# Kernel tuning notes

Measured on AMD Instinct MI355X. Metric: run time of the kernel, lower is better.

Reference implementation:

```python
import jax, jax.numpy as jnp
import numpy as np

N_EMBD = 2048
N_HEAD = 16
N_KV_HEAD = 4
HEAD_DIM = 128
KV_REPEATS = N_HEAD // N_KV_HEAD
ROPE_THETA = 10000.0


def rotate_half(x):
    # interleaved pair rotation: (x0,x1,x2,x3,...) -> (-x1,x0,-x3,x2,...)
    x_even = x[..., 0::2]
    x_odd = x[..., 1::2]
    return jnp.stack((-x_odd, x_even), axis=-1).reshape(x.shape)


def apply_rope(q, k, position_ids):
    inv_freq = 1.0 / (ROPE_THETA ** (jnp.arange(0, HEAD_DIM, 2, dtype=jnp.float32) / HEAD_DIM))
    freqs = position_ids.astype(jnp.float32)[:, None] * inv_freq[None, :]  # [S, D/2]
    emb = jnp.repeat(freqs, 2, axis=-1)  # [S, D] interleaved
    cos = jnp.cos(emb)[None, None, :, :]
    sin = jnp.sin(emb)[None, None, :, :]
    return q * cos + rotate_half(q) * sin, k * cos + rotate_half(k) * sin


def setup_inputs() -> dict:
    key = jax.random.key(0)
    ks = jax.random.split(key, 5)
    B, S = 2, 2048
    x = jax.random.normal(ks[0], (B, S, N_EMBD), dtype=jnp.float32)
    position_ids = jnp.arange(S, dtype=jnp.int32)
    scale = 0.02
    Wq = jax.random.normal(ks[1], (N_HEAD * HEAD_DIM, N_EMBD), dtype=jnp.float32) * scale
    Wk = jax.random.normal(ks[2], (N_KV_HEAD * HEAD_DIM, N_EMBD), dtype=jnp.float32) * scale
    Wv = jax.random.normal(ks[3], (N_KV_HEAD * HEAD_DIM, N_EMBD), dtype=jnp.float32) * scale
    Wo = jax.random.normal(ks[4], (N_EMBD, N_EMBD), dtype=jnp.float32) * scale
    return {"x": x, "Wq": Wq, "Wk": Wk, "Wv": Wv, "Wo": Wo, "position_ids": position_ids}


def reference(x, Wq, Wk, Wv, Wo, position_ids):
    B, S, _ = x.shape
    q = (x @ Wq.T).reshape(B, S, N_HEAD, HEAD_DIM).transpose(0, 2, 1, 3)      # [B,H,S,D]
    k = (x @ Wk.T).reshape(B, S, N_KV_HEAD, HEAD_DIM).transpose(0, 2, 1, 3)  # [B,Hkv,S,D]
    v = (x @ Wv.T).reshape(B, S, N_KV_HEAD, HEAD_DIM).transpose(0, 2, 1, 3)
    q, k = apply_rope(q, k, position_ids)
    # GQA: repeat kv heads consecutively
    k = jnp.repeat(k, KV_REPEATS, axis=1)  # [B,H,S,D]
    v = jnp.repeat(v, KV_REPEATS, axis=1)
    scores = jnp.einsum('bhqd,bhkd->bhqk', q, k) / jnp.sqrt(jnp.asarray(HEAD_DIM, q.dtype))
    key_positions = jnp.arange(S)
    mask = key_positions[None, :] > position_ids[:, None]  # [S, S]
    scores = jnp.where(mask[None, None, :, :], jnp.finfo(scores.dtype).min, scores)
    weights = jax.nn.softmax(scores.astype(jnp.float32), axis=-1).astype(q.dtype)
    y = jnp.einsum('bhqk,bhkd->bhqd', weights, v)
    y = y.transpose(0, 2, 1, 3).reshape(B, S, N_EMBD)
    return y @ Wo.T
```

## Files before the change

### kernel.cpp

```cpp
#include <hip/hip_runtime.h>
#include <stdint.h>

typedef unsigned short u16;
typedef unsigned int   u32;
typedef __attribute__((ext_vector_type(8))) short short8;
typedef __attribute__((ext_vector_type(4))) float f32x4;

#define S_LEN 2048
#define NEMB  2048
#define NH    16
#define NKV   4
#define HD    128
#define BATCH 2
#define MROWS (BATCH*S_LEN)

__device__ __forceinline__ u16 f2bf(float f){
  u32 u = __float_as_uint(f);
  u += 0x7fffu + ((u>>16)&1u);
  return (u16)(u>>16);
}
__device__ __forceinline__ float bf2f(u16 h){
  return __uint_as_float(((u32)h)<<16);
}

typedef __attribute__((address_space(1))) const void gc_void;
typedef __attribute__((address_space(3))) void lds_void;
__device__ __forceinline__ void load_lds16(const void* g, void* l){
  __builtin_amdgcn_global_load_lds((gc_void*)(uintptr_t)g,
      (lds_void*)(u32)(uintptr_t)l, 16, 0, 0);
}

__global__ __launch_bounds__(256) void convert_kernel(
    const float* __restrict__ x, const float* __restrict__ wq,
    const float* __restrict__ wk, const float* __restrict__ wv,
    const float* __restrict__ wo,
    u16* __restrict__ xb, u16* __restrict__ wcb, u16* __restrict__ wob){
  const size_t NX=2097152, NWQ=1048576, NWK=262144, NWV=262144, NWO=1048576;
  const size_t total = NX+NWQ+NWK+NWV+NWO;
  for (size_t i = (size_t)blockIdx.x*blockDim.x + threadIdx.x; i < total;
       i += (size_t)gridDim.x*blockDim.x){
    const float* src; u16* dst; size_t j = i;
    if (j < NX){ src=x; dst=xb; }
    else { j-=NX;
      if (j<NWQ){ src=wq; dst=wcb; }
      else { j-=NWQ;
        if (j<NWK){ src=wk; dst=wcb+4194304; }
        else { j-=NWK;
          if (j<NWV){ src=wv; dst=wcb+5242880; }
          else { j-=NWV; src=wo; dst=wob; } } } }
    float4 v = *(const float4*)(src + j*4);
    u32 lo = (u32)f2bf(v.x) | ((u32)f2bf(v.y)<<16);
    u32 hi = (u32)f2bf(v.z) | ((u32)f2bf(v.w)<<16);
    uint2 pk; pk.x = lo; pk.y = hi;
    *(uint2*)(dst + j*4) = pk;
  }
}

__global__ __launch_bounds__(256) void rope_table_kernel(const int* __restrict__ pos,
                                                         float* __restrict__ tab){
  int id = blockIdx.x*256 + threadIdx.x;
  if (id >= S_LEN*64) return;
  int s = id >> 6, i = id & 63;
  float p = (float)pos[s];
  float inv = __expf(-((float)(2*i)) * (1.0f/128.0f) * 9.210340371976184f);
  float f = p * inv;
  float sv, cv;
  sincosf(f, &sv, &cv);
  tab[id*2]   = cv;
  tab[id*2+1] = sv;
}

__global__ __launch_bounds__(256) void rope_apply_kernel(u16* __restrict__ buf,
    const float* __restrict__ tab, int cols, int cshift, float scale){
  int nch = MROWS * (cols>>3);
  int stride = gridDim.x*blockDim.x;
  for (int ch = blockIdx.x*blockDim.x + threadIdx.x; ch < nch; ch += stride){
    int m   = ch >> cshift;
    int cc  = ch & ((1<<cshift)-1);
    int col = cc<<3;
    int d   = col & (HD-1);
    int i0  = d >> 1;
    int s   = m & (S_LEN-1);
    const float* tp = tab + (size_t)(s*64 + i0)*2;
    float4 t0 = *(const float4*)tp;
    float4 t1 = *(const float4*)(tp+4);
    u16* bp = buf + (size_t)m*cols + col;
    union { uint4 v; u16 e[8]; } U, O;
    U.v = *(const uint4*)bp;
    float a, b;
    a=bf2f(U.e[0]); b=bf2f(U.e[1]);
    O.e[0]=f2bf((a*t0.x - b*t0.y)*scale); O.e[1]=f2bf((b*t0.x + a*t0.y)*scale);
    a=bf2f(U.e[2]); b=bf2f(U.e[3]);
    O.e[2]=f2bf((a*t0.z - b*t0.w)*scale); O.e[3]=f2bf((b*t0.z + a*t0.w)*scale);
    a=bf2f(U.e[4]); b=bf2f(U.e[5]);
    O.e[4]=f2bf((a*t1.x - b*t1.y)*scale); O.e[5]=f2bf((b*t1.x + a*t1.y)*scale);
    a=bf2f(U.e[6]); b=bf2f(U.e[7]);
    O.e[6]=f2bf((a*t1.z - b*t1.w)*scale); O.e[7]=f2bf((b*t1.z + a*t1.w)*scale);
    *(uint4*)bp = O.v;
  }
}

__global__ __launch_bounds__(256) void transpose_v_kernel(const u16* __restrict__ vb,
                                                          u16* __restrict__ vt){
  __shared__ u16 tl[64][72];
  int bx = blockIdx.x;
  int m0 = (bx & 63)*64;
  int d0 = (bx >> 6)*64;
  int tid = threadIdx.x;
  #pragma unroll
  for (int i=0;i<2;i++){
    int t16 = i*256 + tid;
    int sl = t16 >> 3, dc = t16 & 7;
    *(uint4*)&tl[sl][dc*8] = *(const uint4*)&vb[(size_t)(m0+sl)*512 + d0 + dc*8];
  }
  __syncthreads();
  #pragma unroll
  for (int i=0;i<2;i++){
    int t16 = i*256 + tid;
    int sch = t16 >> 6, dl = t16 & 63;
    union { uint4 v; u16 e[8]; } O;
    #pragma unroll
    for (int j=0;j<8;j++) O.e[j] = tl[sch*8+j][dl];
    *(uint4*)&vt[(size_t)(d0+dl)*4096 + m0 + sch*8] = O.v;
  }
}

template<int EPI>
__global__ __launch_bounds__(256,2) void gemm128_kernel(
    const u16* __restrict__ A, const u16* __restrict__ B, int K,
    u16* __restrict__ q_out, u16* __restrict__ k_out, u16* __restrict__ v_out,
    float* __restrict__ f_out){
  __shared__ u16 sA[2][128*32];
  __shared__ u16 sB[2][128*32];
  int tid = threadIdx.x;
  int wave = tid >> 6, lane = tid & 63;
  int lr = lane & 15, lc = lane >> 4;
  int wm = (wave>>1)*64, wn = (wave&1)*64;
  int bm = blockIdx.y*128, bn = blockIdx.x*128;
  const u16* Ag = A + (size_t)bm*K;
  const u16* Bg = B + (size_t)bn*K;

  auto stage = [&](int buf, int kt){
    const u16* Ak = Ag + kt*32;
    const u16* Bk = Bg + kt*32;
    #pragma unroll
    for (int rrd=0; rrd<2; ++rrd){
      int t16 = rrd*256 + tid;
      int row = t16 >> 2, ch = t16 & 3;
      u16* lb = &sA[buf][(size_t)(rrd*256 + (tid & 192))*8];
      load_lds16(Ak + (size_t)row*K + ch*8, lb);
    }
    #pragma unroll
    for (int rrd=0; rrd<2; ++rrd){
      int t16 = rrd*256 + tid;
      int row = t16 >> 2, ch = t16 & 3;
      u16* lb = &sB[buf][(size_t)(rrd*256 + (tid & 192))*8];
      load_lds16(Bk + (size_t)row*K + ch*8, lb);
    }
  };

  f32x4 acc[4][4];
  #pragma unroll
  for (int i=0;i<4;i++)
    #pragma unroll
    for (int j=0;j<4;j++) acc[i][j] = (f32x4)0.0f;

  stage(0,0);
  __syncthreads();
  int nk = K >> 5;
  int cur = 0;
  for (int kt=0; kt<nk; ++kt){
    if (kt+1 < nk) stage(cur^1, kt+1);
    short8 af[4], bfr[4];
    #pragma unroll
    for (int i=0;i<4;i++){
      af[i]  = *(const short8*)&sA[cur][(wm + i*16 + lr)*32 + lc*8];
      bfr[i] = *(const short8*)&sB[cur][(wn + i*16 + lr)*32 + lc*8];
    }
    __builtin_amdgcn_s_setprio(1);
    #pragma unroll
    for (int i=0;i<4;i++)
      #pragma unroll
      for (int j=0;j<4;j++)
        acc[i][j] = __builtin_amdgcn_mfma_f32_16x16x32_bf16(af[i], bfr[j], acc[i][j], 0,0,0);
    __builtin_amdgcn_s_setprio(0);
    __syncthreads();
    cur ^= 1;
  }

  #pragma unroll
  for (int i=0;i<4;i++){
    #pragma unroll
    for (int j=0;j<4;j++){
      #pragma unroll
      for (int r=0;r<4;r++){
        int m = bm + wm + i*16 + lc*4 + r;
        int n = bn + wn + j*16 + lr;
        float v = acc[i][j][r];
        if (EPI == 0){
          if (n < 2048)      q_out[(size_t)m*2048 + n]        = f2bf(v);
          else if (n < 2560) k_out[(size_t)m*512 + (n-2048)]  = f2bf(v);
          else               v_out[(size_t)m*512 + (n-2560)]  = f2bf(v);
        } else {
          f_out[(size_t)m*2048 + n] = v;
        }
      }
    }
  }
}

__global__ __launch_bounds__(256,2) void attn_kernel(
    const u16* __restrict__ Q, const u16* __restrict__ Kb,
    const u16* __restrict__ Vt, u16* __restrict__ Y){
  __shared__ u16 sK[2][64*128];
  __shared__ u16 sVt[2][128*64];
  __shared__ u16 sP[4][16*64];

  int tid = threadIdx.x, wave = tid>>6, lane = tid&63;
  int lr = lane&15, lc = lane>>4;

  int bid = blockIdx.x;
  int kvg  = bid & 7;
  int rest = bid >> 3;
  int qtr  = rest & 31;
  int hsub = rest >> 5;
  int qt = 31 - qtr;
  int b  = kvg >> 2;
  int hk = kvg & 3;
  int h  = hk*4 + hsub;

  int q0  = qt*64;
  int qrb = q0 + wave*16;
  const u16* Qg = Q  + (size_t)(b*S_LEN + qrb)*NEMB + h*HD;
  const u16* Kg = Kb + (size_t)(b*S_LEN)*512 + hk*HD;
  const u16* Vg = Vt + (size_t)(hk*HD)*4096 + b*S_LEN;

  auto stage = [&](int buf, int kv0){
    #pragma unroll
    for (int i=0;i<4;i++){
      int t16 = i*256 + tid;
      int row = t16 >> 4, c = t16 & 15;
      int cgl = c ^ (row & 7);
      load_lds16(Kg + (size_t)(kv0+row)*512 + cgl*8,
                 &sK[buf][(size_t)(i*256 + (tid & 192))*8]);
    }
    #pragma unroll
    for (int i=0;i<4;i++){
      int t16 = i*256 + tid;
      int d = t16 >> 3, c = t16 & 7;
      int cgl = c ^ (d & 7);
      load_lds16(Vg + (size_t)d*4096 + kv0 + cgl*8,
                 &sVt[buf][(size_t)(i*256 + (tid & 192))*8]);
    }
  };

  short8 qf[4];
  #pragma unroll
  for (int c=0;c<4;c++)
    qf[c] = *(const short8*)&Qg[(size_t)lr*NEMB + c*32 + lc*8];

  float m_run[4], l_run[4];
  #pragma unroll
  for (int r=0;r<4;r++){ m_run[r]=-1e30f; l_run[r]=0.0f; }
  f32x4 o[8];
  #pragma unroll
  for (int i=0;i<8;i++) o[i]=(f32x4)0.0f;

  int nt = qt + 1;
  stage(0,0);
  __syncthreads();
  int cur=0;
  char* spb = (char*)sP[wave];
  for (int t=0;t<nt;++t){
    int kv0 = t*64;
    if (t+1<nt) stage(cur^1,(t+1)*64);

    f32x4 sc[4];
    #pragma unroll
    for (int c2=0;c2<4;c2++) sc[c2]=(f32x4)0.0f;
    const char* skb = (const char*)sK[cur];
    __builtin_amdgcn_s_setprio(1);
    #pragma unroll
    for (int c2=0;c2<4;c2++){
      int rr = c2*16 + lr;
      int xo = (rr&7)<<4;
      #pragma unroll
      for (int c=0;c<4;c++){
        int byteoff = (rr*256 + c*64 + lc*16) ^ xo;
        short8 kf = *(const short8*)(skb + byteoff);
        sc[c2] = __builtin_amdgcn_mfma_f32_16x16x32_bf16(qf[c], kf, sc[c2], 0,0,0);
      }
    }
    __builtin_amdgcn_s_setprio(0);

    if (t == nt-1){
      #pragma unroll
      for (int c2=0;c2<4;c2++){
        int kvgl = kv0 + c2*16 + lr;
        #pragma unroll
        for (int r=0;r<4;r++){
          int qg = qrb + lc*4 + r;
          if (kvgl > qg) sc[c2][r] = -1e30f;
        }
      }
    }

    float fac[4];
    #pragma unroll
    for (int r=0;r<4;r++){
      float mm = fmaxf(fmaxf(sc[0][r],sc[1][r]), fmaxf(sc[2][r],sc[3][r]));
      mm = fmaxf(mm, __shfl_xor(mm,1));
      mm = fmaxf(mm, __shfl_xor(mm,2));
      mm = fmaxf(mm, __shfl_xor(mm,4));
      mm = fmaxf(mm, __shfl_xor(mm,8));
      float mn = fmaxf(m_run[r], mm);
      fac[r] = __expf(m_run[r]-mn);
      m_run[r] = mn;
      float p0 = __expf(sc[0][r]-mn);
      float p1 = __expf(sc[1][r]-mn);
      float p2 = __expf(sc[2][r]-mn);
      float p3 = __expf(sc[3][r]-mn);
      sc[0][r]=p0; sc[1][r]=p1; sc[2][r]=p2; sc[3][r]=p3;
      float ss = (p0+p1)+(p2+p3);
      ss += __shfl_xor(ss,1); ss += __shfl_xor(ss,2);
      ss += __shfl_xor(ss,4); ss += __shfl_xor(ss,8);
      l_run[r] = l_run[r]*fac[r] + ss;
    }
    #pragma unroll
    for (int i=0;i<8;i++)
      #pragma unroll
      for (int r=0;r<4;r++) o[i][r] *= fac[r];

    #pragma unroll
    for (int c2=0;c2<4;c2++){
      #pragma unroll
      for (int r=0;r<4;r++){
        int row = lc*4+r;
        int byteoff = (row*128 + (c2*16+lr)*2) ^ ((row&7)<<4);
        *(u16*)(spb + byteoff) = f2bf(sc[c2][r]);
      }
    }
    short8 pa[2];
    {
      int xop = (lr&7)<<4;
      pa[0] = *(const short8*)(spb + ((lr*128 + lc*16) ^ xop));
      pa[1] = *(const short8*)(spb + ((lr*128 + 64 + lc*16) ^ xop));
    }

    const char* svb = (const char*)sVt[cur];
    __builtin_amdgcn_s_setprio(1);
    #pragma unroll
    for (int n=0;n<8;n++){
      int d = n*16+lr;
      int xo = (d&7)<<4;
      #pragma unroll
      for (int ks=0;ks<2;ks++){
        int byteoff = (d*128 + ks*64 + lc*16) ^ xo;
        short8 vf = *(const short8*)(svb + byteoff);
        o[n] = __builtin_amdgcn_mfma_f32_16x16x32_bf16(pa[ks], vf, o[n], 0,0,0);
      }
    }
    __builtin_amdgcn_s_setprio(0);

    __syncthreads();
    cur ^= 1;
  }

  u16* Yg = Y + (size_t)(b*S_LEN + qrb)*NEMB + h*HD;
  #pragma unroll
  for (int n=0;n<8;n++){
    #pragma unroll
    for (int r=0;r<4;r++){
      float v = o[n][r] / l_run[r];
      Yg[(size_t)(lc*4+r)*NEMB + n*16 + lr] = f2bf(v);
    }
  }
}

extern "C" void kernel_launch(void* const* d_in, const int* in_sizes, int n_in,
                              void* d_out, int out_size, void* d_ws, size_t ws_size,
                              hipStream_t stream){
  const float* x  = (const float*)d_in[0];
  const float* wq = (const float*)d_in[1];
  const float* wk = (const float*)d_in[2];
  const float* wv = (const float*)d_in[3];
  const float* wo = (const float*)d_in[4];
  const int*  pos = (const int*)d_in[5];
  float* out = (float*)d_out;

  char* ws = (char*)d_ws;
  size_t off = 0;
  auto alloc = [&](size_t bytes)->char*{
    char* p = ws + off; off += (bytes + 255) & ~(size_t)255; return p;
  };
  u16* xb  = (u16*)alloc(8388608ull*2);
  u16* wcb = (u16*)alloc(6291456ull*2);
  u16* wob = (u16*)alloc(4194304ull*2);
  u16* qb  = (u16*)alloc(8388608ull*2);
  u16* kb  = (u16*)alloc(2097152ull*2);
  u16* vb  = (u16*)alloc(2097152ull*2);
  u16* yb  = (u16*)alloc(8388608ull*2);
  float* tab = (float*)alloc((size_t)S_LEN*64*2*4);
  u16* vt = xb;

  convert_kernel<<<2048,256,0,stream>>>(x,wq,wk,wv,wo,xb,wcb,wob);
  rope_table_kernel<<<512,256,0,stream>>>(pos, tab);
  gemm128_kernel<0><<<dim3(24,32),256,0,stream>>>(xb, wcb, 2048, qb, kb, vb, nullptr);
  rope_apply_kernel<<<2048,256,0,stream>>>(qb, tab, 2048, 8, 0.08838834764831845f);
  rope_apply_kernel<<<1024,256,0,stream>>>(kb, tab, 512, 6, 1.0f);
  transpose_v_kernel<<<512,256,0,stream>>>(vb, vt);
  attn_kernel<<<1024,256,0,stream>>>(qb, kb, vt, yb);
  gemm128_kernel<1><<<dim3(16,32),256,0,stream>>>(yb, wob, 2048, nullptr,nullptr,nullptr, out);
}
```

Measured before the change: 360.6 us.

## Replace 128x128 GEMM with 256x256 tiled, swizzled, quarter-pipelined GEMM

After: 386.0 us. 1.07x slower.

```diff
diff --git a/kernel.cpp b/kernel.cpp
--- a/kernel.cpp
+++ b/kernel.cpp
@@ -126,77 +126,170 @@
 }
 
 template<int EPI>
-__global__ __launch_bounds__(256,2) void gemm128_kernel(
-    const u16* __restrict__ A, const u16* __restrict__ B, int K,
+__global__ __launch_bounds__(512,1) void gemm256_kernel(
+    const u16* __restrict__ A, const u16* __restrict__ B, int K, int ntx,
     u16* __restrict__ q_out, u16* __restrict__ k_out, u16* __restrict__ v_out,
     float* __restrict__ f_out){
-  __shared__ u16 sA[2][128*32];
-  __shared__ u16 sB[2][128*32];
+  __shared__ char ldsb[131072];
   int tid = threadIdx.x;
-  int wave = tid >> 6, lane = tid & 63;
+  int lane = tid & 63;
+  int wid  = tid >> 6;
   int lr = lane & 15, lc = lane >> 4;
-  int wm = (wave>>1)*64, wn = (wave&1)*64;
-  int bm = blockIdx.y*128, bn = blockIdx.x*128;
+  int wm2 = wid >> 2;
+  int wn4 = wid & 3;
+
+  int nwg = ntx * 16;
+  int bid = blockIdx.x;
+  int wg = (bid & 7)*(nwg >> 3) + (bid >> 3);
+  int by = wg / ntx, bx = wg % ntx;
+  int bm = by*256, bn = bx*256;
+
   const u16* Ag = A + (size_t)bm*K;
   const u16* Bg = B + (size_t)bn*K;
 
-  auto stage = [&](int buf, int kt){
-    const u16* Ak = Ag + kt*32;
-    const u16* Bk = Bg + kt*32;
-    #pragma unroll
-    for (int rrd=0; rrd<2; ++rrd){
-      int t16 = rrd*256 + tid;
-      int row = t16 >> 2, ch = t16 & 3;
-      u16* lb = &sA[buf][(size_t)(rrd*256 + (tid & 192))*8];
-      load_lds16(Ak + (size_t)row*K + ch*8, lb);
-    }
-    #pragma unroll
-    for (int rrd=0; rrd<2; ++rrd){
-      int t16 = rrd*256 + tid;
-      int row = t16 >> 2, ch = t16 & 3;
-      u16* lb = &sB[buf][(size_t)(rrd*256 + (tid & 192))*8];
-      load_lds16(Bk + (size_t)row*K + ch*8, lb);
+  auto stageA = [&](int p, int kt, int h){
+    const u16* src = Ag + (size_t)kt*64;
+    char* dstb = ldsb + p*32768 + h*16384 + (size_t)(tid & 448)*16;
+    #pragma unroll
+    for (int i=0;i<2;i++){
+      int S = i*512 + tid;
+      int rr = S >> 3;
+      int r  = ((rr>>6)<<7) | (h<<6) | (rr & 63);
+      int c8 = (S & 7) ^ (rr & 7);
+      load_lds16(src + (size_t)r*K + c8*8, dstb + i*8192);
     }
   };
-
-  f32x4 acc[4][4];
-  #pragma unroll
-  for (int i=0;i<4;i++)
+  auto stageB = [&](int p, int kt, int h){
+    const u16* src = Bg + (size_t)kt*64;
+    char* dstb = ldsb + 65536 + p*32768 + h*16384 + (size_t)(tid & 448)*16;
+    #pragma unroll
+    for (int i=0;i<2;i++){
+      int S = i*512 + tid;
+      int rr = S >> 3;
+      int n  = ((rr>>5)<<6) | (h<<5) | (rr & 31);
+      int c8 = (S & 7) ^ (rr & 7);
+      load_lds16(src + (size_t)n*K + c8*8, dstb + i*8192);
+    }
+  };
+
+  f32x4 acc[8][4];
+  #pragma unroll
+  for (int i=0;i<8;i++)
     #pragma unroll
     for (int j=0;j<4;j++) acc[i][j] = (f32x4)0.0f;
 
-  stage(0,0);
-  __syncthreads();
-  int nk = K >> 5;
-  int cur = 0;
-  for (int kt=0; kt<nk; ++kt){
-    if (kt+1 < nk) stage(cur^1, kt+1);
-    short8 af[4], bfr[4];
-    #pragma unroll
-    for (int i=0;i<4;i++){
-      af[i]  = *(const short8*)&sA[cur][(wm + i*16 + lr)*32 + lc*8];
-      bfr[i] = *(const short8*)&sB[cur][(wn + i*16 + lr)*32 + lc*8];
-    }
+  short8 a[4][2], b0[2][2], b1[2][2];
+  int xorv = (lr & 7) << 4;
+
+  #define RD_A(mh, mf, kk, p) \
+    (*(const short8*)(ldsb + (p)*32768 + (mh)*16384 + wm2*8192 + \
+      ((((mf)*16 + lr)*128 + (kk)*64 + lc*16) ^ xorv)))
+  #define RD_B(nh, nf, kk, p) \
+    (*(const short8*)(ldsb + 65536 + (p)*32768 + (nh)*16384 + wn4*4096 + \
+      ((((nf)*16 + lr)*128 + (kk)*64 + lc*16) ^ xorv)))
+
+  int nk = K >> 6;
+
+  stageA(0, 0, 0);
+  stageB(0, 0, 0);
+  stageB(0, 0, 1);
+  stageA(0, 0, 1);
+  asm volatile("s_waitcnt vmcnt(4)" ::: "memory");
+  __builtin_amdgcn_s_barrier();
+
+  for (int t = 0; t < nk; ++t){
+    int p = t & 1;
+    bool doStage = (t+1 < nk);
+
+    #pragma unroll
+    for (int mf=0; mf<4; mf++){
+      a[mf][0] = RD_A(0, mf, 0, p);
+      a[mf][1] = RD_A(0, mf, 1, p);
+    }
+    #pragma unroll
+    for (int nf=0; nf<2; nf++){
+      b0[nf][0] = RD_B(0, nf, 0, p);
+      b0[nf][1] = RD_B(0, nf, 1, p);
+    }
+    if (doStage) stageA(p^1, t+1, 0);
+    __builtin_amdgcn_s_barrier();
     __builtin_amdgcn_s_setprio(1);
     #pragma unroll
-    for (int i=0;i<4;i++)
-      #pragma unroll
-      for (int j=0;j<4;j++)
-        acc[i][j] = __builtin_amdgcn_mfma_f32_16x16x32_bf16(af[i], bfr[j], acc[i][j], 0,0,0);
+    for (int kk=0; kk<2; kk++)
+      #pragma unroll
+      for (int mf=0; mf<4; mf++)
+        #pragma unroll
+        for (int nf=0; nf<2; nf++)
+          acc[mf][nf] = __builtin_amdgcn_mfma_f32_16x16x32_bf16(a[mf][kk], b0[nf][kk], acc[mf][nf], 0,0,0);
     __builtin_amdgcn_s_setprio(0);
-    __syncthreads();
-    cur ^= 1;
-  }
-
-  #pragma unroll
-  for (int i=0;i<4;i++){
-    #pragma unroll
-    for (int j=0;j<4;j++){
-      #pragma unroll
-      for (int r=0;r<4;r++){
-        int m = bm + wm + i*16 + lc*4 + r;
-        int n = bn + wn + j*16 + lr;
-        float v = acc[i][j][r];
+    if (doStage) { asm volatile("s_waitcnt vmcnt(4)" ::: "memory"); }
+    else         { asm volatile("s_waitcnt vmcnt(2)" ::: "memory"); }
+    __builtin_amdgcn_s_barrier();
+
+    #pragma unroll
+    for (int nf=0; nf<2; nf++){
+      b1[nf][0] = RD_B(1, nf, 0, p);
+      b1[nf][1] = RD_B(1, nf, 1, p);
+    }
+    if (doStage) stageB(p^1, t+1, 0);
+    __builtin_amdgcn_s_barrier();
+    __builtin_amdgcn_s_setprio(1);
+    #pragma unroll
+    for (int kk=0; kk<2; kk++)
+      #pragma unroll
+      for (int mf=0; mf<4; mf++)
+        #pragma unroll
+        for (int nf=0; nf<2; nf++)
+          acc[mf][2+nf] = __builtin_amdgcn_mfma_f32_16x16x32_bf16(a[mf][kk], b1[nf][kk], acc[mf][2+nf], 0,0,0);
+    __builtin_amdgcn_s_setprio(0);
+    if (doStage) { asm volatile("s_waitcnt vmcnt(4)" ::: "memory"); }
+    else         { asm volatile("s_waitcnt vmcnt(0)" ::: "memory"); }
+    __builtin_amdgcn_s_barrier();
+
+    #pragma unroll
+    for (int mf=0; mf<4; mf++){
+      a[mf][0] = RD_A(1, mf, 0, p);
+      a[mf][1] = RD_A(1, mf, 1, p);
+    }
+    if (doStage) stageB(p^1, t+1, 1);
+    __builtin_amdgcn_s_barrier();
+    __builtin_amdgcn_s_setprio(1);
+    #pragma unroll
+    for (int kk=0; kk<2; kk++)
+      #pragma unroll
+      for (int mf=0; mf<4; mf++)
+        #pragma unroll
+        for (int nf=0; nf<2; nf++)
+          acc[4+mf][nf] = __builtin_amdgcn_mfma_f32_16x16x32_bf16(a[mf][kk], b0[nf][kk], acc[4+mf][nf], 0,0,0);
+    __builtin_amdgcn_s_setprio(0);
+    __builtin_amdgcn_s_barrier();
+
+    if (doStage) stageA(p^1, t+1, 1);
+    __builtin_amdgcn_s_barrier();
+    __builtin_amdgcn_s_setprio(1);
+    #pragma unroll
+    for (int kk=0; kk<2; kk++)
+      #pragma unroll
+      for (int mf=0; mf<4; mf++)
+        #pragma unroll
+        for (int nf=0; nf<2; nf++)
+          acc[4+mf][2+nf] = __builtin_amdgcn_mfma_f32_16x16x32_bf16(a[mf][kk], b1[nf][kk], acc[4+mf][2+nf], 0,0,0);
+    __builtin_amdgcn_s_setprio(0);
+    if (doStage) { asm volatile("s_waitcnt vmcnt(4)" ::: "memory"); }
+    __builtin_amdgcn_s_barrier();
+  }
+  #undef RD_A
+  #undef RD_B
+
+  #pragma unroll
+  for (int mfi=0; mfi<8; mfi++){
+    #pragma unroll
+    for (int nfi=0; nfi<4; nfi++){
+      #pragma unroll
+      for (int r=0; r<4; r++){
+        int m = bm + wm2*128 + mfi*16 + lc*4 + r;
+        int n = bn + wn4*64 + nfi*16 + lr;
+        float v = acc[mfi][nfi][r];
         if (EPI == 0){
           if (n < 2048)      q_out[(size_t)m*2048 + n]        = f2bf(v);
           else if (n < 2560) k_out[(size_t)m*512 + (n-2048)]  = f2bf(v);
@@ -405,10 +498,10 @@
 
   convert_kernel<<<2048,256,0,stream>>>(x,wq,wk,wv,wo,xb,wcb,wob);
   rope_table_kernel<<<512,256,0,stream>>>(pos, tab);
-  gemm128_kernel<0><<<dim3(24,32),256,0,stream>>>(xb, wcb, 2048, qb, kb, vb, nullptr);
+  gemm256_kernel<0><<<192,512,0,stream>>>(xb, wcb, 2048, 12, qb, kb, vb, nullptr);
   rope_apply_kernel<<<2048,256,0,stream>>>(qb, tab, 2048, 8, 0.08838834764831845f);
   rope_apply_kernel<<<1024,256,0,stream>>>(kb, tab, 512, 6, 1.0f);
   transpose_v_kernel<<<512,256,0,stream>>>(vb, vt);
   attn_kernel<<<1024,256,0,stream>>>(qb, kb, vt, yb);
-  gemm128_kernel<1><<<dim3(16,32),256,0,stream>>>(yb, wob, 2048, nullptr,nullptr,nullptr, out);
-}
+  gemm256_kernel<1><<<128,512,0,stream>>>(yb, wob, 2048, 8, nullptr,nullptr,nullptr, out);
+}
```

## Fuse RoPE into QKV GEMM epilogue and use exp2 with lazy softmax rescaling

Applied to the files above, without the earlier changes.

Result: faster. 349.3 us (-3.1%).

```diff
diff --git a/kernel.cpp b/kernel.cpp
--- a/kernel.cpp
+++ b/kernel.cpp
@@ -14,6 +14,8 @@
 #define BATCH 2
 #define MROWS (BATCH*S_LEN)
 
+#define SCALE_Q 0.12751744f
+
 __device__ __forceinline__ u16 f2bf(float f){
   u32 u = __float_as_uint(f);
   u += 0x7fffu + ((u>>16)&1u);
@@ -21,6 +23,11 @@
 }
 __device__ __forceinline__ float bf2f(u16 h){
   return __uint_as_float(((u32)h)<<16);
+}
+__device__ __forceinline__ float exp2_fast(float x){
+  float r;
+  asm("v_exp_f32 %0, %1" : "=v"(r) : "v"(x));
+  return r;
 }
 
 typedef __attribute__((address_space(1))) const void gc_void;
@@ -57,7 +64,7 @@
 }
 
 __global__ __launch_bounds__(256) void rope_table_kernel(const int* __restrict__ pos,
-                                                         float* __restrict__ tab){
+                                                         float2* __restrict__ tab){
   int id = blockIdx.x*256 + threadIdx.x;
   if (id >= S_LEN*64) return;
   int s = id >> 6, i = id & 63;
@@ -66,38 +73,7 @@
   float f = p * inv;
   float sv, cv;
   sincosf(f, &sv, &cv);
-  tab[id*2]   = cv;
-  tab[id*2+1] = sv;
-}
-
-__global__ __launch_bounds__(256) void rope_apply_kernel(u16* __restrict__ buf,
-    const float* __restrict__ tab, int cols, int cshift, float scale){
-  int nch = MROWS * (cols>>3);
-  int stride = gridDim.x*blockDim.x;
-  for (int ch = blockIdx.x*blockDim.x + threadIdx.x; ch < nch; ch += stride){
-    int m   = ch >> cshift;
-    int cc  = ch & ((1<<cshift)-1);
-    int col = cc<<3;
-    int d   = col & (HD-1);
-    int i0  = d >> 1;
-    int s   = m & (S_LEN-1);
-    const float* tp = tab + (size_t)(s*64 + i0)*2;
-    float4 t0 = *(const float4*)tp;
-    float4 t1 = *(const float4*)(tp+4);
-    u16* bp = buf + (size_t)m*cols + col;
-    union { uint4 v; u16 e[8]; } U, O;
-    U.v = *(const uint4*)bp;
-    float a, b;
-    a=bf2f(U.e[0]); b=bf2f(U.e[1]);
-    O.e[0]=f2bf((a*t0.x - b*t0.y)*scale); O.e[1]=f2bf((b*t0.x + a*t0.y)*scale);
-    a=bf2f(U.e[2]); b=bf2f(U.e[3]);
-    O.e[2]=f2bf((a*t0.z - b*t0.w)*scale); O.e[3]=f2bf((b*t0.z + a*t0.w)*scale);
-    a=bf2f(U.e[4]); b=bf2f(U.e[5]);
-    O.e[4]=f2bf((a*t1.x - b*t1.y)*scale); O.e[5]=f2bf((b*t1.x + a*t1.y)*scale);
-    a=bf2f(U.e[6]); b=bf2f(U.e[7]);
-    O.e[6]=f2bf((a*t1.z - b*t1.w)*scale); O.e[7]=f2bf((b*t1.z + a*t1.w)*scale);
-    *(uint4*)bp = O.v;
-  }
+  tab[id] = make_float2(cv, sv);
 }
 
 __global__ __launch_bounds__(256) void transpose_v_kernel(const u16* __restrict__ vb,
@@ -128,6 +104,7 @@
 template<int EPI>
 __global__ __launch_bounds__(256,2) void gemm128_kernel(
     const u16* __restrict__ A, const u16* __restrict__ B, int K,
+    const float2* __restrict__ tab,
     u16* __restrict__ q_out, u16* __restrict__ k_out, u16* __restrict__ v_out,
     float* __restrict__ f_out){
   __shared__ u16 sA[2][128*32];
@@ -198,9 +175,19 @@
         int n = bn + wn + j*16 + lr;
         float v = acc[i][j][r];
         if (EPI == 0){
-          if (n < 2048)      q_out[(size_t)m*2048 + n]        = f2bf(v);
-          else if (n < 2560) k_out[(size_t)m*512 + (n-2048)]  = f2bf(v);
-          else               v_out[(size_t)m*512 + (n-2560)]  = f2bf(v);
+          float p = __shfl_xor(v, 1);
+          if (n < 2048){
+            float2 cs = tab[((m & (S_LEN-1))<<6) + ((n & 127)>>1)];
+            float o = (n & 1) ? (v*cs.x + p*cs.y) : (v*cs.x - p*cs.y);
+            q_out[(size_t)m*2048 + n] = f2bf(o * SCALE_Q);
+          } else if (n < 2560){
+            int d = n - 2048;
+            float2 cs = tab[((m & (S_LEN-1))<<6) + ((d & 127)>>1)];
+            float o = (n & 1) ? (v*cs.x + p*cs.y) : (v*cs.x - p*cs.y);
+            k_out[(size_t)m*512 + d] = f2bf(o);
+          } else {
+            v_out[(size_t)m*512 + (n-2560)] = f2bf(v);
+          }
         } else {
           f_out[(size_t)m*2048 + n] = v;
         }
@@ -305,31 +292,44 @@
       }
     }
 
-    float fac[4];
+    float lmax[4];
+    bool need = false;
     #pragma unroll
     for (int r=0;r<4;r++){
-      float mm = fmaxf(fmaxf(sc[0][r],sc[1][r]), fmaxf(sc[2][r],sc[3][r]));
-      mm = fmaxf(mm, __shfl_xor(mm,1));
-      mm = fmaxf(mm, __shfl_xor(mm,2));
-      mm = fmaxf(mm, __shfl_xor(mm,4));
-      mm = fmaxf(mm, __shfl_xor(mm,8));
-      float mn = fmaxf(m_run[r], mm);
-      fac[r] = __expf(m_run[r]-mn);
-      m_run[r] = mn;
-      float p0 = __expf(sc[0][r]-mn);
-      float p1 = __expf(sc[1][r]-mn);
-      float p2 = __expf(sc[2][r]-mn);
-      float p3 = __expf(sc[3][r]-mn);
+      lmax[r] = fmaxf(fmaxf(sc[0][r],sc[1][r]), fmaxf(sc[2][r],sc[3][r]));
+      need = need || (lmax[r] > m_run[r] + 8.0f);
+    }
+    if (__any(need)){
+      float fac[4];
+      #pragma unroll
+      for (int r=0;r<4;r++){
+        float mm = lmax[r];
+        mm = fmaxf(mm, __shfl_xor(mm,1));
+        mm = fmaxf(mm, __shfl_xor(mm,2));
+        mm = fmaxf(mm, __shfl_xor(mm,4));
+        mm = fmaxf(mm, __shfl_xor(mm,8));
+        float mn = fmaxf(m_run[r], mm);
+        fac[r] = exp2_fast(m_run[r]-mn);
+        m_run[r] = mn;
+        l_run[r] *= fac[r];
+      }
+      #pragma unroll
+      for (int i=0;i<8;i++)
+        #pragma unroll
+        for (int r=0;r<4;r++) o[i][r] *= fac[r];
+    }
+    #pragma unroll
+    for (int r=0;r<4;r++){
+      float p0 = exp2_fast(sc[0][r]-m_run[r]);
+      float p1 = exp2_fast(sc[1][r]-m_run[r]);
+      float p2 = exp2_fast(sc[2][r]-m_run[r]);
+      float p3 = exp2_fast(sc[3][r]-m_run[r]);
       sc[0][r]=p0; sc[1][r]=p1; sc[2][r]=p2; sc[3][r]=p3;
       float ss = (p0+p1)+(p2+p3);
       ss += __shfl_xor(ss,1); ss += __shfl_xor(ss,2);
       ss += __shfl_xor(ss,4); ss += __shfl_xor(ss,8);
-      l_run[r] = l_run[r]*fac[r] + ss;
-    }
-    #pragma unroll
-    for (int i=0;i<8;i++)
-      #pragma unroll
-      for (int r=0;r<4;r++) o[i][r] *= fac[r];
+      l_run[r] += ss;
+    }
 
     #pragma unroll
     for (int c2=0;c2<4;c2++){
@@ -400,15 +400,13 @@
   u16* kb  = (u16*)alloc(2097152ull*2);
   u16* vb  = (u16*)alloc(2097152ull*2);
   u16* yb  = (u16*)alloc(8388608ull*2);
-  float* tab = (float*)alloc((size_t)S_LEN*64*2*4);
+  float2* tab = (float2*)alloc((size_t)S_LEN*64*8);
   u16* vt = xb;
 
   convert_kernel<<<2048,256,0,stream>>>(x,wq,wk,wv,wo,xb,wcb,wob);
   rope_table_kernel<<<512,256,0,stream>>>(pos, tab);
-  gemm128_kernel<0><<<dim3(24,32),256,0,stream>>>(xb, wcb, 2048, qb, kb, vb, nullptr);
-  rope_apply_kernel<<<2048,256,0,stream>>>(qb, tab, 2048, 8, 0.08838834764831845f);
-  rope_apply_kernel<<<1024,256,0,stream>>>(kb, tab, 512, 6, 1.0f);
+  gemm128_kernel<0><<<dim3(24,32),256,0,stream>>>(xb, wcb, 2048, tab, qb, kb, vb, nullptr);
   transpose_v_kernel<<<512,256,0,stream>>>(vb, vt);
   attn_kernel<<<1024,256,0,stream>>>(qb, kb, vt, yb);
-  gemm128_kernel<1><<<dim3(16,32),256,0,stream>>>(yb, wob, 2048, nullptr,nullptr,nullptr, out);
-}
+  gemm128_kernel<1><<<dim3(16,32),256,0,stream>>>(yb, wob, 2048, nullptr, nullptr,nullptr,nullptr, out);
+}
```
